# Kernel tuning notes

Hardware: AMD Instinct MI355X
Metric: run time of the kernel (lower is better)

The kernel has to match this reference:

```python
import jax, jax.numpy as jnp
import numpy as np

B = 16384
T = 64  # num_taps

def setup_inputs() -> dict:
    key = jax.random.key(0)
    k1, k2 = jax.random.split(key)
    x = jax.random.normal(k1, (B, T), dtype=jnp.float32)
    d = jax.random.normal(k2, (B,), dtype=jnp.float32)
    w_prev = jnp.zeros((B, T), dtype=jnp.float32)
    # standard RLS init: P0 = delta * I, batched
    P_prev = jnp.broadcast_to(jnp.eye(T, dtype=jnp.float32), (B, T, T))
    forgetting_factor = jnp.asarray(0.99, dtype=jnp.float32)
    return {"x": x, "d": d, "w_prev": w_prev, "P_prev": P_prev,
            "forgetting_factor": forgetting_factor}

def reference(x, d, w_prev, P_prev, forgetting_factor):
    lam = jnp.clip(forgetting_factor, 0.0001, 0.9999)
    # Px = P_prev @ x  -> (B, T)
    Px = jnp.einsum('bij,bj->bi', P_prev, x)
    # denom = lambda + x^T P x  -> (B,)
    denom = lam + jnp.einsum('bi,bi->b', x, Px)
    g = Px / denom[:, None]                         # gain (B, T)
    y_hat = jnp.sum(w_prev * x, axis=-1)            # (B,)
    error = d - y_hat
    w_next = w_prev + g * error[:, None]
    # P_update = g (x^T P_prev)  -> rank-1 (B, T, T)
    xP = jnp.einsum('bi,bij->bj', x, P_prev)
    P_next = (P_prev - g[:, :, None] * xP[:, None, :]) / lam
    return (w_next, P_next, y_hat)
```

## Files before the change

kernel.cpp:

```cpp
#include <hip/hip_runtime.h>


constexpr int T = 64;

__global__ __launch_bounds__(256) void rls_step(
    const float* __restrict__ x,
    const float* __restrict__ d,
    const float* __restrict__ w_prev,
    const float* __restrict__ P_prev,
    const float* __restrict__ ffp,
    float* __restrict__ w_next,
    float* __restrict__ P_next,
    float* __restrict__ y_hat)
{
    const int b    = blockIdx.x;
    const int t    = threadIdx.x;
    const int lane = t & 63;

    __shared__ float x_s[T];
    __shared__ float w_s[T];
    __shared__ float Px_s[T];
    __shared__ float xP_part[16][T];
    __shared__ float xP_s[T];
    __shared__ float g_s[T];
    __shared__ float sc[2];

    const float lam     = fminf(fmaxf(ffp[0], 1.0e-4f), 0.9999f);
    const float inv_lam = 1.0f / lam;

    const float4* __restrict__ Pv  =
        reinterpret_cast<const float4*>(P_prev) + (size_t)b * (T * T / 4);
    float4* __restrict__ Pnv =
        reinterpret_cast<float4*>(P_next) + (size_t)b * (T * T / 4);

    float4 p0 = Pv[0 * 256 + t];
    float4 p1 = Pv[1 * 256 + t];
    float4 p2 = Pv[2 * 256 + t];
    float4 p3 = Pv[3 * 256 + t];

    if (t < T)            x_s[t]     = x[(size_t)b * T + t];
    else if (t < 2 * T)   w_s[t - T] = w_prev[(size_t)b * T + (t - T)];
    __syncthreads();

    const int grp = t >> 4;
    const int c0  = (t & 15) * 4;

    const float xc0 = x_s[c0 + 0], xc1 = x_s[c0 + 1];
    const float xc2 = x_s[c0 + 2], xc3 = x_s[c0 + 3];

    {
        float part;
        part = p0.x * xc0 + p0.y * xc1 + p0.z * xc2 + p0.w * xc3;
        part += __shfl_xor(part, 1); part += __shfl_xor(part, 2);
        part += __shfl_xor(part, 4); part += __shfl_xor(part, 8);
        if ((t & 15) == 0) Px_s[grp + 0]  = part;
        part = p1.x * xc0 + p1.y * xc1 + p1.z * xc2 + p1.w * xc3;
        part += __shfl_xor(part, 1); part += __shfl_xor(part, 2);
        part += __shfl_xor(part, 4); part += __shfl_xor(part, 8);
        if ((t & 15) == 0) Px_s[grp + 16] = part;
        part = p2.x * xc0 + p2.y * xc1 + p2.z * xc2 + p2.w * xc3;
        part += __shfl_xor(part, 1); part += __shfl_xor(part, 2);
        part += __shfl_xor(part, 4); part += __shfl_xor(part, 8);
        if ((t & 15) == 0) Px_s[grp + 32] = part;
        part = p3.x * xc0 + p3.y * xc1 + p3.z * xc2 + p3.w * xc3;
        part += __shfl_xor(part, 1); part += __shfl_xor(part, 2);
        part += __shfl_xor(part, 4); part += __shfl_xor(part, 8);
        if ((t & 15) == 0) Px_s[grp + 48] = part;
    }

    {
        const float xi0 = x_s[grp +  0];
        const float xi1 = x_s[grp + 16];
        const float xi2 = x_s[grp + 32];
        const float xi3 = x_s[grp + 48];
        float s0 = xi0 * p0.x + xi1 * p1.x + xi2 * p2.x + xi3 * p3.x;
        float s1 = xi0 * p0.y + xi1 * p1.y + xi2 * p2.y + xi3 * p3.y;
        float s2 = xi0 * p0.z + xi1 * p1.z + xi2 * p2.z + xi3 * p3.z;
        float s3 = xi0 * p0.w + xi1 * p1.w + xi2 * p2.w + xi3 * p3.w;
        *reinterpret_cast<float4*>(&xP_part[grp][c0]) = make_float4(s0, s1, s2, s3);
    }
    __syncthreads();

    if (t < 64) {
        float s = 0.0f;
        #pragma unroll
        for (int gg = 0; gg < 16; ++gg) s += xP_part[gg][t];
        xP_s[t] = s;
    } else if (t < 128) {
        float v = x_s[lane] * Px_s[lane];
        v += __shfl_xor(v, 1);  v += __shfl_xor(v, 2);  v += __shfl_xor(v, 4);
        v += __shfl_xor(v, 8);  v += __shfl_xor(v, 16); v += __shfl_xor(v, 32);
        if (lane == 0) sc[0] = 1.0f / (lam + v);
    } else if (t < 192) {
        float v = w_s[lane] * x_s[lane];
        v += __shfl_xor(v, 1);  v += __shfl_xor(v, 2);  v += __shfl_xor(v, 4);
        v += __shfl_xor(v, 8);  v += __shfl_xor(v, 16); v += __shfl_xor(v, 32);
        if (lane == 0) {
            y_hat[b] = v;
            sc[1]    = d[b] - v;
        }
    }
    __syncthreads();

    if (t < 64) {
        const float gj = Px_s[t] * sc[0];
        g_s[t] = gj;
        w_next[(size_t)b * T + t] = w_s[t] + gj * sc[1];
    }
    __syncthreads();

    {
        const float xq0 = xP_s[c0 + 0], xq1 = xP_s[c0 + 1];
        const float xq2 = xP_s[c0 + 2], xq3 = xP_s[c0 + 3];
        const float g0 = g_s[grp +  0];
        const float g1 = g_s[grp + 16];
        const float g2 = g_s[grp + 32];
        const float g3 = g_s[grp + 48];
        float4 o;
        o.x = (p0.x - g0 * xq0) * inv_lam;
        o.y = (p0.y - g0 * xq1) * inv_lam;
        o.z = (p0.z - g0 * xq2) * inv_lam;
        o.w = (p0.w - g0 * xq3) * inv_lam;
        Pnv[0 * 256 + t] = o;
        o.x = (p1.x - g1 * xq0) * inv_lam;
        o.y = (p1.y - g1 * xq1) * inv_lam;
        o.z = (p1.z - g1 * xq2) * inv_lam;
        o.w = (p1.w - g1 * xq3) * inv_lam;
        Pnv[1 * 256 + t] = o;
        o.x = (p2.x - g2 * xq0) * inv_lam;
        o.y = (p2.y - g2 * xq1) * inv_lam;
        o.z = (p2.z - g2 * xq2) * inv_lam;
        o.w = (p2.w - g2 * xq3) * inv_lam;
        Pnv[2 * 256 + t] = o;
        o.x = (p3.x - g3 * xq0) * inv_lam;
        o.y = (p3.y - g3 * xq1) * inv_lam;
        o.z = (p3.z - g3 * xq2) * inv_lam;
        o.w = (p3.w - g3 * xq3) * inv_lam;
        Pnv[3 * 256 + t] = o;
    }
}

extern "C" void kernel_launch(void* const* d_in, const int* in_sizes, int n_in,
                              void* d_out, int out_size, void* d_ws, size_t ws_size,
                              hipStream_t stream) {
    const float* x      = (const float*)d_in[0];
    const float* d      = (const float*)d_in[1];
    const float* w_prev = (const float*)d_in[2];
    const float* P_prev = (const float*)d_in[3];
    const float* ffp    = (const float*)d_in[4];

    const int B = in_sizes[1];

    float* out    = (float*)d_out;
    float* w_next = out;
    float* P_next = out + (size_t)B * T;
    float* y_hat  = out + (size_t)B * T + (size_t)B * T * T;

    rls_step<<<B, 256, 0, stream>>>(x, d, w_prev, P_prev, ffp,
                                    w_next, P_next, y_hat);
}
```

Before: 101.8 us.

## Cut block barriers from four to two via register-held partial reductions

Restructures the per-batch RLS kernel so Px, the denominator x^T P x, xP and y_hat are all reduced with wave shuffles in one pass and kept in registers. Only per-wave partials go through shared memory, which removes two of the four __syncthreads and the 16-way shared xP reduction. It also uses vectorised x/w loads. The workload is memory bound (16384 x 64x64 floats read and written), so removing barriers mostly shortens latency per block and may not change DRAM-bound time much.

New measurement: 102.5 us. About the same (+0.7%).

```diff
diff --git a/kernel.cpp b/kernel.cpp
--- a/kernel.cpp
+++ b/kernel.cpp
@@ -15,20 +15,23 @@
 {
     const int b    = blockIdx.x;
     const int t    = threadIdx.x;
+    const int wave = t >> 6;
     const int lane = t & 63;
+    const int grp  = t >> 4;
+    const int sub  = t & 15;
+    const int c0   = sub * 4;
 
-    __shared__ float x_s[T];
-    __shared__ float w_s[T];
-    __shared__ float Px_s[T];
-    __shared__ float xP_part[16][T];
-    __shared__ float xP_s[T];
-    __shared__ float g_s[T];
-    __shared__ float sc[2];
+    __shared__ float  x_s[T];
+    __shared__ float  w_s[T];
+    __shared__ float  Px_s[T];
+    __shared__ float4 xPw[4][16];
+    __shared__ float  denw[4];
 
     const float lam     = fminf(fmaxf(ffp[0], 1.0e-4f), 0.9999f);
     const float inv_lam = 1.0f / lam;
+    const float db      = d[b];
 
-    const float4* __restrict__ Pv  =
+    const float4* __restrict__ Pv =
         reinterpret_cast<const float4*>(P_prev) + (size_t)b * (T * T / 4);
     float4* __restrict__ Pnv =
         reinterpret_cast<float4*>(P_next) + (size_t)b * (T * T / 4);
@@ -38,106 +41,104 @@
     float4 p2 = Pv[2 * 256 + t];
     float4 p3 = Pv[3 * 256 + t];
 
-    if (t < T)            x_s[t]     = x[(size_t)b * T + t];
-    else if (t < 2 * T)   w_s[t - T] = w_prev[(size_t)b * T + (t - T)];
+    if (t < 16)
+        reinterpret_cast<float4*>(x_s)[t] =
+            reinterpret_cast<const float4*>(x + (size_t)b * T)[t];
+    else if (t < 32)
+        reinterpret_cast<float4*>(w_s)[t - 16] =
+            reinterpret_cast<const float4*>(w_prev + (size_t)b * T)[t - 16];
     __syncthreads();
-
-    const int grp = t >> 4;
-    const int c0  = (t & 15) * 4;
 
     const float xc0 = x_s[c0 + 0], xc1 = x_s[c0 + 1];
     const float xc2 = x_s[c0 + 2], xc3 = x_s[c0 + 3];
+    const float xi0 = x_s[grp +  0];
+    const float xi1 = x_s[grp + 16];
+    const float xi2 = x_s[grp + 32];
+    const float xi3 = x_s[grp + 48];
 
-    {
-        float part;
-        part = p0.x * xc0 + p0.y * xc1 + p0.z * xc2 + p0.w * xc3;
-        part += __shfl_xor(part, 1); part += __shfl_xor(part, 2);
-        part += __shfl_xor(part, 4); part += __shfl_xor(part, 8);
-        if ((t & 15) == 0) Px_s[grp + 0]  = part;
-        part = p1.x * xc0 + p1.y * xc1 + p1.z * xc2 + p1.w * xc3;
-        part += __shfl_xor(part, 1); part += __shfl_xor(part, 2);
-        part += __shfl_xor(part, 4); part += __shfl_xor(part, 8);
-        if ((t & 15) == 0) Px_s[grp + 16] = part;
-        part = p2.x * xc0 + p2.y * xc1 + p2.z * xc2 + p2.w * xc3;
-        part += __shfl_xor(part, 1); part += __shfl_xor(part, 2);
-        part += __shfl_xor(part, 4); part += __shfl_xor(part, 8);
-        if ((t & 15) == 0) Px_s[grp + 32] = part;
-        part = p3.x * xc0 + p3.y * xc1 + p3.z * xc2 + p3.w * xc3;
-        part += __shfl_xor(part, 1); part += __shfl_xor(part, 2);
-        part += __shfl_xor(part, 4); part += __shfl_xor(part, 8);
-        if ((t & 15) == 0) Px_s[grp + 48] = part;
+    float r0 = p0.x * xc0 + p0.y * xc1 + p0.z * xc2 + p0.w * xc3;
+    float r1 = p1.x * xc0 + p1.y * xc1 + p1.z * xc2 + p1.w * xc3;
+    float r2 = p2.x * xc0 + p2.y * xc1 + p2.z * xc2 + p2.w * xc3;
+    float r3 = p3.x * xc0 + p3.y * xc1 + p3.z * xc2 + p3.w * xc3;
+
+    float dpart = xi0 * r0 + xi1 * r1 + xi2 * r2 + xi3 * r3;
+
+    float yp = w_s[lane] * x_s[lane];
+
+    r0 += __shfl_xor(r0, 1); r0 += __shfl_xor(r0, 2); r0 += __shfl_xor(r0, 4); r0 += __shfl_xor(r0, 8);
+    r1 += __shfl_xor(r1, 1); r1 += __shfl_xor(r1, 2); r1 += __shfl_xor(r1, 4); r1 += __shfl_xor(r1, 8);
+    r2 += __shfl_xor(r2, 1); r2 += __shfl_xor(r2, 2); r2 += __shfl_xor(r2, 4); r2 += __shfl_xor(r2, 8);
+    r3 += __shfl_xor(r3, 1); r3 += __shfl_xor(r3, 2); r3 += __shfl_xor(r3, 4); r3 += __shfl_xor(r3, 8);
+    if (sub == 0) {
+        Px_s[grp +  0] = r0;
+        Px_s[grp + 16] = r1;
+        Px_s[grp + 32] = r2;
+        Px_s[grp + 48] = r3;
     }
 
-    {
-        const float xi0 = x_s[grp +  0];
-        const float xi1 = x_s[grp + 16];
-        const float xi2 = x_s[grp + 32];
-        const float xi3 = x_s[grp + 48];
-        float s0 = xi0 * p0.x + xi1 * p1.x + xi2 * p2.x + xi3 * p3.x;
-        float s1 = xi0 * p0.y + xi1 * p1.y + xi2 * p2.y + xi3 * p3.y;
-        float s2 = xi0 * p0.z + xi1 * p1.z + xi2 * p2.z + xi3 * p3.z;
-        float s3 = xi0 * p0.w + xi1 * p1.w + xi2 * p2.w + xi3 * p3.w;
-        *reinterpret_cast<float4*>(&xP_part[grp][c0]) = make_float4(s0, s1, s2, s3);
-    }
+    float s0 = xi0 * p0.x + xi1 * p1.x + xi2 * p2.x + xi3 * p3.x;
+    float s1 = xi0 * p0.y + xi1 * p1.y + xi2 * p2.y + xi3 * p3.y;
+    float s2 = xi0 * p0.z + xi1 * p1.z + xi2 * p2.z + xi3 * p3.z;
+    float s3 = xi0 * p0.w + xi1 * p1.w + xi2 * p2.w + xi3 * p3.w;
+    s0 += __shfl_xor(s0, 16); s0 += __shfl_xor(s0, 32);
+    s1 += __shfl_xor(s1, 16); s1 += __shfl_xor(s1, 32);
+    s2 += __shfl_xor(s2, 16); s2 += __shfl_xor(s2, 32);
+    s3 += __shfl_xor(s3, 16); s3 += __shfl_xor(s3, 32);
+    if (lane < 16) xPw[wave][lane] = make_float4(s0, s1, s2, s3);
+
+    dpart += __shfl_xor(dpart, 1);  dpart += __shfl_xor(dpart, 2);
+    dpart += __shfl_xor(dpart, 4);  dpart += __shfl_xor(dpart, 8);
+    dpart += __shfl_xor(dpart, 16); dpart += __shfl_xor(dpart, 32);
+    if (lane == 0) denw[wave] = dpart;
+
+    yp += __shfl_xor(yp, 1);  yp += __shfl_xor(yp, 2);
+    yp += __shfl_xor(yp, 4);  yp += __shfl_xor(yp, 8);
+    yp += __shfl_xor(yp, 16); yp += __shfl_xor(yp, 32);
+    const float err = db - yp;
+
     __syncthreads();
 
-    if (t < 64) {
-        float s = 0.0f;
-        #pragma unroll
-        for (int gg = 0; gg < 16; ++gg) s += xP_part[gg][t];
-        xP_s[t] = s;
-    } else if (t < 128) {
-        float v = x_s[lane] * Px_s[lane];
-        v += __shfl_xor(v, 1);  v += __shfl_xor(v, 2);  v += __shfl_xor(v, 4);
-        v += __shfl_xor(v, 8);  v += __shfl_xor(v, 16); v += __shfl_xor(v, 32);
-        if (lane == 0) sc[0] = 1.0f / (lam + v);
-    } else if (t < 192) {
-        float v = w_s[lane] * x_s[lane];
-        v += __shfl_xor(v, 1);  v += __shfl_xor(v, 2);  v += __shfl_xor(v, 4);
-        v += __shfl_xor(v, 8);  v += __shfl_xor(v, 16); v += __shfl_xor(v, 32);
-        if (lane == 0) {
-            y_hat[b] = v;
-            sc[1]    = d[b] - v;
-        }
-    }
-    __syncthreads();
+    const float inv_den = 1.0f / (lam + denw[0] + denw[1] + denw[2] + denw[3]);
+
+    const float4 q0 = xPw[0][sub], q1 = xPw[1][sub];
+    const float4 q2 = xPw[2][sub], q3 = xPw[3][sub];
+    const float xq0 = q0.x + q1.x + q2.x + q3.x;
+    const float xq1 = q0.y + q1.y + q2.y + q3.y;
+    const float xq2 = q0.z + q1.z + q2.z + q3.z;
+    const float xq3 = q0.w + q1.w + q2.w + q3.w;
+
+    const float g0 = r0 * inv_den;
+    const float g1 = r1 * inv_den;
+    const float g2 = r2 * inv_den;
+    const float g3 = r3 * inv_den;
 
     if (t < 64) {
-        const float gj = Px_s[t] * sc[0];
-        g_s[t] = gj;
-        w_next[(size_t)b * T + t] = w_s[t] + gj * sc[1];
+        w_next[(size_t)b * T + t] = w_s[t] + Px_s[t] * inv_den * err;
+    } else if (t == 64) {
+        y_hat[b] = yp;
     }
-    __syncthreads();
 
-    {
-        const float xq0 = xP_s[c0 + 0], xq1 = xP_s[c0 + 1];
-        const float xq2 = xP_s[c0 + 2], xq3 = xP_s[c0 + 3];
-        const float g0 = g_s[grp +  0];
-        const float g1 = g_s[grp + 16];
-        const float g2 = g_s[grp + 32];
-        const float g3 = g_s[grp + 48];
-        float4 o;
-        o.x = (p0.x - g0 * xq0) * inv_lam;
-        o.y = (p0.y - g0 * xq1) * inv_lam;
-        o.z = (p0.z - g0 * xq2) * inv_lam;
-        o.w = (p0.w - g0 * xq3) * inv_lam;
-        Pnv[0 * 256 + t] = o;
-        o.x = (p1.x - g1 * xq0) * inv_lam;
-        o.y = (p1.y - g1 * xq1) * inv_lam;
-        o.z = (p1.z - g1 * xq2) * inv_lam;
-        o.w = (p1.w - g1 * xq3) * inv_lam;
-        Pnv[1 * 256 + t] = o;
-        o.x = (p2.x - g2 * xq0) * inv_lam;
-        o.y = (p2.y - g2 * xq1) * inv_lam;
-        o.z = (p2.z - g2 * xq2) * inv_lam;
-        o.w = (p2.w - g2 * xq3) * inv_lam;
-        Pnv[2 * 256 + t] = o;
-        o.x = (p3.x - g3 * xq0) * inv_lam;
-        o.y = (p3.y - g3 * xq1) * inv_lam;
-        o.z = (p3.z - g3 * xq2) * inv_lam;
-        o.w = (p3.w - g3 * xq3) * inv_lam;
-        Pnv[3 * 256 + t] = o;
-    }
+    float4 o;
+    o.x = (p0.x - g0 * xq0) * inv_lam;
+    o.y = (p0.y - g0 * xq1) * inv_lam;
+    o.z = (p0.z - g0 * xq2) * inv_lam;
+    o.w = (p0.w - g0 * xq3) * inv_lam;
+    Pnv[0 * 256 + t] = o;
+    o.x = (p1.x - g1 * xq0) * inv_lam;
+    o.y = (p1.y - g1 * xq1) * inv_lam;
+    o.z = (p1.z - g1 * xq2) * inv_lam;
+    o.w = (p1.w - g1 * xq3) * inv_lam;
+    Pnv[1 * 256 + t] = o;
+    o.x = (p2.x - g2 * xq0) * inv_lam;
+    o.y = (p2.y - g2 * xq1) * inv_lam;
+    o.z = (p2.z - g2 * xq2) * inv_lam;
+    o.w = (p2.w - g2 * xq3) * inv_lam;
+    Pnv[2 * 256 + t] = o;
+    o.x = (p3.x - g3 * xq0) * inv_lam;
+    o.y = (p3.y - g3 * xq1) * inv_lam;
+    o.z = (p3.z - g3 * xq2) * inv_lam;
+    o.w = (p3.w - g3 * xq3) * inv_lam;
+    Pnv[3 * 256 + t] = o;
 }
 
 extern "C" void kernel_launch(void* const* d_in, const int* in_sizes, int n_in,
```
